# Optimization experiments

Hardware: AMD Instinct MI355X
Metric: run time of the kernel (lower is better)

Reference implementation:

```python
import jax, jax.numpy as jnp
import numpy as np


def _lstm_cell(x, h, c, Wih, Whh, bih, bhh):
    # PyTorch LSTMCell gate order: i, f, g, o
    g = x @ Wih.T + h @ Whh.T + bih + bhh
    i, f, gg, o = jnp.split(g, 4, axis=-1)
    c = jax.nn.sigmoid(f) * c + jax.nn.sigmoid(i) * jnp.tanh(gg)
    h = jax.nn.sigmoid(o) * jnp.tanh(c)
    return h, c


def setup_inputs() -> dict:
    F, H, B, Te, Td = 64, 128, 1024, 168, 24
    shapes = {
        'input_p_q': (B, Te, F), 'label_p': (B, Td),
        'Wi_w': (H, F), 'Wi_b': (H,), 'We_w': (H, 2 * H),
        'Vd_w': (F, H), 'Vd_b': (F,),
        'enc_Wih': (4 * H, F), 'enc_Whh': (4 * H, H), 'enc_bih': (4 * H,), 'enc_bhh': (4 * H,),
        'mid_Wih': (4 * H, H), 'mid_Whh': (4 * H, H), 'mid_bih': (4 * H,), 'mid_bhh': (4 * H,),
        'Wx_w': (H, H), 'Wx_b': (H,), 'Wh_w': (H, 2 * H),
        'V_w': (1, H), 'V_b': (1,),
        'dec_Wih': (4 * H, H), 'dec_Whh': (4 * H, H), 'dec_bih': (4 * H,), 'dec_bhh': (4 * H,),
        'reg_w': (1, H), 'reg_b': (1,),
    }
    key = jax.random.key(0)
    ks = jax.random.split(key, len(shapes))
    out = {}
    for k, (name, shp) in zip(ks, shapes.items()):
        scale = 1.0 if name in ('input_p_q', 'label_p') else 0.05
        out[name] = jax.random.normal(k, shp, jnp.float32) * scale
    return out


def reference(input_p_q, label_p, Wi_w, Wi_b, We_w, Vd_w, Vd_b,
              enc_Wih, enc_Whh, enc_bih, enc_bhh,
              mid_Wih, mid_Whh, mid_bih, mid_bhh,
              Wx_w, Wx_b, Wh_w, V_w, V_b,
              dec_Wih, dec_Whh, dec_bih, dec_bhh, reg_w, reg_b):
    B, Te, F = input_p_q.shape
    H = Wi_w.shape[0]
    Td = label_p.shape[1]
    h0 = jnp.zeros((B, H), input_p_q.dtype)

    # ---- spatial-attention LSTMCell encoder ----
    xs = jnp.transpose(input_p_q, (1, 0, 2))  # [Te, B, F]

    def enc_step(carry, x_t):
        h, c = carry
        s = jnp.tanh(jnp.concatenate([h, c], axis=1) @ We_w.T
                     + x_t @ Wi_w.T + Wi_b) @ Vd_w.T + Vd_b  # [B, F]
        x_in = x_t * jax.nn.softmax(s, axis=1)
        h, c = _lstm_cell(x_in, h, c, enc_Wih, enc_Whh, enc_bih, enc_bhh)
        return (h, c), h

    _, mid = jax.lax.scan(enc_step, (h0, h0), xs)  # [Te, B, H]

    # ---- single-layer nn.LSTM (LSTM_mid), zero init state ----
    def mid_step(carry, x_t):
        h, c = carry
        h, c = _lstm_cell(x_t, h, c, mid_Wih, mid_Whh, mid_bih, mid_bhh)
        return (h, c), h

    (hi, ci), mid_out = jax.lax.scan(mid_step, (h0, h0), mid)
    mid_out = jnp.transpose(mid_out, (1, 0, 2))  # [B, Te, H]

    # ---- temporal-attention LSTMCell decoder (no softmax on scores, faithful) ----
    wx_mid = mid_out @ Wx_w.T + Wx_b  # [B, Te, H]

    def dec_step(carry, _):
        hi, ci = carry
        q = jnp.concatenate([hi, ci], axis=1) @ Wh_w.T  # [B, H]
        s = jnp.tanh(q[:, None, :] + wx_mid) @ V_w.T + V_b  # [B, Te, 1]
        dec_in = jnp.einsum('bt,bth->bh', s[..., 0], mid_out)
        hi, ci = _lstm_cell(dec_in, hi, ci, dec_Wih, dec_Whh, dec_bih, dec_bhh)
        return (hi, ci), hi

    _, dec = jax.lax.scan(dec_step, (hi, ci), None, length=Td)  # [Td, B, H]
    out = jnp.transpose(dec, (1, 0, 2)) @ reg_w.T + reg_b  # [B, Td, 1]
    return out[..., 0]
```

## Files before the change

### kernel.cpp

```cpp
#include <hip/hip_runtime.h>

#define B_   1024
#define TE   168
#define TD   24
#define F_   64
#define H_   128
#define H2_  256
#define G_   512

#define OFF_WhT    0
#define OFF_dWihT  16384
#define OFF_dWhhT  49152
#define OFF_ENCB   81920
#define OFF_MIDB   82432
#define OFF_DECB   82944
#define OFF_W16    83456
#define W16_We     0
#define W16_Wi     32768
#define W16_Vd     40960
#define W16_eWih   49152
#define W16_eWhh   81920
#define W16_mWih   147456
#define W16_mWhh   212992
#define W16_Wx     278528
#define W16_TOT    294912
#define OFF_MID    230912
#define OFF_WX     (OFF_MID + (B_*TE*H_)/2)
#define OFF_STH    (OFF_WX  + (B_*TE*H_)/2)
#define OFF_STC    (OFF_STH + B_*H_)
#define WS_FLOATS  (OFF_STC + B_*H_)

typedef _Float16 h2 __attribute__((ext_vector_type(2)));
typedef _Float16 h8 __attribute__((ext_vector_type(8)));
typedef _Float16 f16x8 __attribute__((ext_vector_type(8)));
typedef float    f32x4 __attribute__((ext_vector_type(4)));

__device__ __forceinline__ float fexp2(float x) { return __builtin_amdgcn_exp2f(x); }
__device__ __forceinline__ float frcp(float x)  { return __builtin_amdgcn_rcpf(x); }
#define LOG2E 1.4426950408889634f

__device__ __forceinline__ float sigm(float x) {
    return frcp(1.f + fexp2(-LOG2E * x));
}
__device__ __forceinline__ float tanh_fast(float x) {
    float e = fexp2(2.f * LOG2E * x);
    return 1.f - 2.f * frcp(e + 1.f);
}

__device__ __forceinline__ float fdot2(h2 a, h2 b, float c) {
#if __has_builtin(__builtin_amdgcn_fdot2)
    return __builtin_amdgcn_fdot2(a, b, c, false);
#else
    return c + (float)a[0] * (float)b[0] + (float)a[1] * (float)b[1];
#endif
}
__device__ __forceinline__ void fma4(float4& g, const float4 wv, const float s) {
    g.x = __builtin_fmaf(wv.x, s, g.x);
    g.y = __builtin_fmaf(wv.y, s, g.y);
    g.z = __builtin_fmaf(wv.z, s, g.z);
    g.w = __builtin_fmaf(wv.w, s, g.w);
}

#define SH(V,I)  __builtin_shufflevector(V, V, 2*(I), 2*(I)+1)
#define SL(CG)   (4*((CG) + ((CG)>>3)))

#define DPAIR2(LOV, HIV, R0, R1) { \
    h2 c0=SH(LOV,0), c1=SH(LOV,1), c2=SH(LOV,2), c3=SH(LOV,3); \
    h2 c4=SH(HIV,0), c5=SH(HIV,1), c6=SH(HIV,2), c7=SH(HIV,3); \
    a00.x=fdot2(R0,c0,a00.x); a00.y=fdot2(R0,c1,a00.y); a00.z=fdot2(R0,c2,a00.z); a00.w=fdot2(R0,c3,a00.w); \
    a01.x=fdot2(R0,c4,a01.x); a01.y=fdot2(R0,c5,a01.y); a01.z=fdot2(R0,c6,a01.z); a01.w=fdot2(R0,c7,a01.w); \
    a10.x=fdot2(R1,c0,a10.x); a10.y=fdot2(R1,c1,a10.y); a10.z=fdot2(R1,c2,a10.z); a10.w=fdot2(R1,c3,a10.w); \
    a11.x=fdot2(R1,c4,a11.x); a11.y=fdot2(R1,c5,a11.y); a11.z=fdot2(R1,c6,a11.z); a11.w=fdot2(R1,c7,a11.w); \
}

__device__ __forceinline__ f32x4 mfma16(f16x8 a, f16x8 b, f32x4 c) {
    return __builtin_amdgcn_mfma_f32_16x16x32_f16(a, b, c, 0, 0, 0);
}

struct PrepArgs {
    const float *We, *Wi, *Vd, *eWih, *eWhh, *eBih, *eBhh,
                *mWih, *mWhh, *mBih, *mBhh, *Wx, *Wh, *dWih, *dWhh, *dBih, *dBhh;
};

__global__ void prep_kernel(PrepArgs a, float* __restrict__ ws) {
    int sec  = blockIdx.x >> 2;
    int base = (blockIdx.x & 3) * blockDim.x + threadIdx.x;
    const int stride = blockDim.x * 4;
    _Float16* w16 = (_Float16*)(ws + OFF_W16);

    if (sec <= 2) {
        const float* src = (sec == 0) ? a.Wh : (sec == 1) ? a.dWih : a.dWhh;
        int R = (sec == 0) ? 128 : 512;
        int C = (sec == 0) ? 256 : 128;
        int off = (sec == 0) ? OFF_WhT : (sec == 1) ? OFF_dWihT : OFF_dWhhT;
        int n = R * C;
        _Float16* hd = (_Float16*)(ws + off);
        for (int o = base; o < n; o += stride) {
            int r = o % R, c = o / R;
            hd[(c >> 1) * 2 * R + 2 * r + (c & 1)] = (_Float16)src[r * C + c];
        }
    } else if (sec == 3) {
        for (int i = base; i < 512; i += stride) ws[OFF_ENCB + i] = a.eBih[i] + a.eBhh[i];
    } else if (sec == 4) {
        for (int i = base; i < 512; i += stride) ws[OFF_MIDB + i] = a.mBih[i] + a.mBhh[i];
    } else if (sec == 5) {
        for (int i = base; i < 512; i += stride) ws[OFF_DECB + i] = a.dBih[i] + a.dBhh[i];
    } else if (sec <= 13) {
        const int dsto[8] = {W16_We, W16_Wi, W16_Vd, W16_eWih, W16_eWhh, W16_mWih, W16_mWhh, W16_Wx};
        const int cnt[8]  = {32768, 8192, 8192, 32768, 65536, 65536, 65536, 16384};
        const float* srcs[8] = {a.We, a.Wi, a.Vd, a.eWih, a.eWhh, a.mWih, a.mWhh, a.Wx};
        int k = sec - 6;
        const float* s = srcs[k];
        _Float16* d = w16 + dsto[k];
        int n = cnt[k];
        for (int i = base; i < n; i += stride) d[i] = (_Float16)s[i];
    }
}

__global__ __launch_bounds__(512, 1) void enc_kernel(
    const float* __restrict__ x_all,
    const float* __restrict__ Wi_b,
    const float* __restrict__ Vd_b,
    float* __restrict__ ws)
{
    __shared__ __align__(16) _Float16 m1In[16][328];
    __shared__ __align__(16) _Float16 encIn[16][200];
    __shared__ __align__(16) _Float16 avT[16][136];
    __shared__ __align__(16) float sS[16][68];
    __shared__ __align__(16) float xf[16][64];
    __shared__ __align__(16) float cE[16][132];
    __shared__ float bWi[H_], bVd[F_], bE[G_];

    const int tid  = threadIdx.x;
    const int wave = tid >> 6;
    const int lane = tid & 63;
    const int g    = lane >> 4;
    const int cc   = lane & 15;
    const int b0   = blockIdx.x * 16;
    const int col  = wave * 16 + cc;

    for (int i = tid; i < 16 * 328; i += 512) ((_Float16*)m1In)[i]  = (_Float16)0.f;
    for (int i = tid; i < 16 * 200; i += 512) ((_Float16*)encIn)[i] = (_Float16)0.f;
    for (int i = tid; i < 16 * 132; i += 512) ((float*)cE)[i] = 0.f;
    if (tid < H_) bWi[tid] = Wi_b[tid];
    if (tid < F_) bVd[tid] = Vd_b[tid];
    bE[tid] = ws[OFF_ENCB + tid];
    if (tid < 256) {
        int m = tid >> 4, c4 = (tid & 15) * 4;
        float4 v = *(const float4*)&x_all[((size_t)(b0 + m) * TE + 0) * F_ + c4];
        *(float4*)&xf[m][c4] = v;
        m1In[m][256 + c4]     = (_Float16)v.x;
        m1In[m][256 + c4 + 1] = (_Float16)v.y;
        m1In[m][256 + c4 + 2] = (_Float16)v.z;
        m1In[m][256 + c4 + 3] = (_Float16)v.w;
    }

    const _Float16* w16 = (const _Float16*)(ws + OFF_W16);
    f16x8 wWe[8], wWi[2], wVd[4], wIh[4][2], wHh[4][4];
    {
        const _Float16* p = w16 + W16_We + (size_t)col * 256 + 8 * g;
        #pragma unroll
        for (int ks = 0; ks < 8; ++ks) wWe[ks] = *(const f16x8*)(p + ks * 32);
        const _Float16* p2 = w16 + W16_Wi + (size_t)col * 64 + 8 * g;
        wWi[0] = *(const f16x8*)(p2);
        wWi[1] = *(const f16x8*)(p2 + 32);
        if (wave < 4) {
            const _Float16* p3 = w16 + W16_Vd + (size_t)col * 128 + 8 * g;
            #pragma unroll
            for (int ks = 0; ks < 4; ++ks) wVd[ks] = *(const f16x8*)(p3 + ks * 32);
        } else {
            #pragma unroll
            for (int ks = 0; ks < 4; ++ks) wVd[ks] = f16x8{};
        }
        #pragma unroll
        for (int q = 0; q < 4; ++q) {
            const _Float16* pi = w16 + W16_eWih + (size_t)(q * 128 + col) * 64 + 8 * g;
            wIh[q][0] = *(const f16x8*)(pi);
            wIh[q][1] = *(const f16x8*)(pi + 32);
            const _Float16* ph = w16 + W16_eWhh + (size_t)(q * 128 + col) * 128 + 8 * g;
            #pragma unroll
            for (int ks = 0; ks < 4; ++ks) wHh[q][ks] = *(const f16x8*)(ph + ks * 32);
        }
    }
    _Float16* hencG = (_Float16*)(ws + OFF_MID);
    __syncthreads();

    float4 xr = make_float4(0.f, 0.f, 0.f, 0.f);

    for (int t = 0; t < TE; ++t) {
        {
            f16x8 aF[10];
            #pragma unroll
            for (int ks = 0; ks < 10; ++ks)
                aF[ks] = *(const f16x8*)&m1In[cc][ks * 32 + 8 * g];
            f32x4 acc = {0.f, 0.f, 0.f, 0.f};
            #pragma unroll
            for (int ks = 0; ks < 8; ++ks)
                acc = mfma16(aF[ks], wWe[ks], acc);
            acc = mfma16(aF[8], wWi[0], acc);
            acc = mfma16(aF[9], wWi[1], acc);
            float bw = bWi[col];
            #pragma unroll
            for (int r = 0; r < 4; ++r)
                avT[4 * g + r][col] = (_Float16)tanh_fast(acc[r] + bw);
        }
        __syncthreads();

        if (wave < 4) {
            f16x8 aF[4];
            #pragma unroll
            for (int ks = 0; ks < 4; ++ks)
                aF[ks] = *(const f16x8*)&avT[cc][ks * 32 + 8 * g];
            f32x4 acc = {0.f, 0.f, 0.f, 0.f};
            #pragma unroll
            for (int ks = 0; ks < 4; ++ks)
                acc = mfma16(aF[ks], wVd[ks], acc);
            float bv = bVd[col];
            #pragma unroll
            for (int r = 0; r < 4; ++r)
                sS[4 * g + r][col] = acc[r] + bv;
        } else if (t + 1 < TE) {
            int q = tid - 256, m = q >> 4, c4 = (q & 15) * 4;
            xr = *(const float4*)&x_all[((size_t)(b0 + m) * TE + (t + 1)) * F_ + c4];
        }
        __syncthreads();

        {
            int m = tid >> 5, c = tid & 31;
            float v0 = sS[m][c], v1 = sS[m][c + 32];
            float mx = fmaxf(v0, v1);
            #pragma unroll
            for (int off = 16; off > 0; off >>= 1) mx = fmaxf(mx, __shfl_xor(mx, off, 64));
            float e0 = fexp2((v0 - mx) * LOG2E);
            float e1 = fexp2((v1 - mx) * LOG2E);
            float sm = e0 + e1;
            #pragma unroll
            for (int off = 16; off > 0; off >>= 1) sm += __shfl_xor(sm, off, 64);
            float rs = frcp(sm);
            encIn[m][c]      = (_Float16)(xf[m][c]      * e0 * rs);
            encIn[m][c + 32] = (_Float16)(xf[m][c + 32] * e1 * rs);
        }
        __syncthreads();

        f32x4 ge[4];
        {
            f16x8 aF[6];
            #pragma unroll
            for (int ks = 0; ks < 6; ++ks)
                aF[ks] = *(const f16x8*)&encIn[cc][ks * 32 + 8 * g];
            #pragma unroll
            for (int q = 0; q < 4; ++q) {
                f32x4 acc = {0.f, 0.f, 0.f, 0.f};
                acc = mfma16(aF[0], wIh[q][0], acc);
                acc = mfma16(aF[1], wIh[q][1], acc);
                #pragma unroll
                for (int ks = 0; ks < 4; ++ks)
                    acc = mfma16(aF[2 + ks], wHh[q][ks], acc);
                ge[q] = acc;
            }
        }
        __syncthreads();
        {
            float bi = bE[col], bf = bE[col + 128], bg = bE[col + 256], bo = bE[col + 384];
            #pragma unroll
            for (int r = 0; r < 4; ++r) {
                int m = 4 * g + r;
                float gi = ge[0][r] + bi, gf = ge[1][r] + bf,
                      gg = ge[2][r] + bg, go = ge[3][r] + bo;
                float cn = sigm(gf) * cE[m][col] + sigm(gi) * tanh_fast(gg);
                float h  = sigm(go) * tanh_fast(cn);
                cE[m][col] = cn;
                _Float16 hh = (_Float16)h;
                encIn[m][64 + col] = hh;
                m1In[m][col]       = hh;
                m1In[m][128 + col] = (_Float16)cn;
                hencG[((size_t)(b0 + m) * TE + t) * H_ + col] = hh;
            }
            if (tid >= 256 && t + 1 < TE) {
                int q = tid - 256, m = q >> 4, c4 = (q & 15) * 4;
                *(float4*)&xf[m][c4] = xr;
                m1In[m][256 + c4]     = (_Float16)xr.x;
                m1In[m][256 + c4 + 1] = (_Float16)xr.y;
                m1In[m][256 + c4 + 2] = (_Float16)xr.z;
                m1In[m][256 + c4 + 3] = (_Float16)xr.w;
            }
        }
        __syncthreads();
    }
}

__global__ __launch_bounds__(512, 1) void mid_kernel(
    const float* __restrict__ Wx_b,
    float* __restrict__ ws)
{
    __shared__ __align__(16) _Float16 midIn[16][264];
    __shared__ __align__(16) float cM[16][132];
    __shared__ float bM[G_], bWx[H_];

    const int tid  = threadIdx.x;
    const int wave = tid >> 6;
    const int lane = tid & 63;
    const int g    = lane >> 4;
    const int cc   = lane & 15;
    const int b0   = blockIdx.x * 16;
    const int col  = wave * 16 + cc;

    for (int i = tid; i < 16 * 264; i += 512) ((_Float16*)midIn)[i] = (_Float16)0.f;
    for (int i = tid; i < 16 * 132; i += 512) ((float*)cM)[i] = 0.f;
    if (tid < H_) bWx[tid] = Wx_b[tid];
    bM[tid] = ws[OFF_MIDB + tid];

    const _Float16* w16 = (const _Float16*)(ws + OFF_W16);
    f16x8 wIhB[4][4], wHhB[4][4], wWx[4];
    {
        #pragma unroll
        for (int q = 0; q < 4; ++q) {
            const _Float16* pi = w16 + W16_mWih + (size_t)(q * 128 + col) * 128 + 8 * g;
            const _Float16* ph = w16 + W16_mWhh + (size_t)(q * 128 + col) * 128 + 8 * g;
            #pragma unroll
            for (int ks = 0; ks < 4; ++ks) {
                wIhB[q][ks] = *(const f16x8*)(pi + ks * 32);
                wHhB[q][ks] = *(const f16x8*)(ph + ks * 32);
            }
        }
        const _Float16* px = w16 + W16_Wx + (size_t)col * 128 + 8 * g;
        #pragma unroll
        for (int ks = 0; ks < 4; ++ks) wWx[ks] = *(const f16x8*)(px + ks * 32);
    }

    _Float16* hencG = (_Float16*)(ws + OFF_MID);
    _Float16* wxH   = (_Float16*)(ws + OFF_WX);
    __syncthreads();

    if (tid < 256) {
        int m = tid >> 4, s8 = (tid & 15) * 8;
        *(f16x8*)&midIn[m][s8] = *(const f16x8*)&hencG[((size_t)(b0 + m) * TE + 0) * H_ + s8];
    }
    __syncthreads();

    f16x8 hpre = {};
    f32x4 accx = {0.f, 0.f, 0.f, 0.f};

    for (int t = 0; t < TE; ++t) {
        f32x4 gm[4];
        {
            f16x8 aF[8];
            #pragma unroll
            for (int ks = 0; ks < 8; ++ks)
                aF[ks] = *(const f16x8*)&midIn[cc][ks * 32 + 8 * g];
            #pragma unroll
            for (int q = 0; q < 4; ++q) {
                f32x4 acc = {0.f, 0.f, 0.f, 0.f};
                #pragma unroll
                for (int ks = 0; ks < 4; ++ks)
                    acc = mfma16(aF[ks], wIhB[q][ks], acc);
                #pragma unroll
                for (int ks = 0; ks < 4; ++ks)
                    acc = mfma16(aF[4 + ks], wHhB[q][ks], acc);
                gm[q] = acc;
            }
            if (t > 0) {
                f32x4 acc = {0.f, 0.f, 0.f, 0.f};
                #pragma unroll
                for (int ks = 0; ks < 4; ++ks)
                    acc = mfma16(aF[4 + ks], wWx[ks], acc);
                accx = acc;
            }
        }
        if (tid < 256 && t + 1 < TE) {
            int m = tid >> 4, s8 = (tid & 15) * 8;
            hpre = *(const f16x8*)&hencG[((size_t)(b0 + m) * TE + (t + 1)) * H_ + s8];
        }
        __syncthreads();

        {
            float bi = bM[col], bf = bM[col + 128], bg = bM[col + 256], bo = bM[col + 384];
            float bw = bWx[col];
            #pragma unroll
            for (int r = 0; r < 4; ++r) {
                int m = 4 * g + r;
                float gi = gm[0][r] + bi, gf = gm[1][r] + bf,
                      gg = gm[2][r] + bg, go = gm[3][r] + bo;
                float cn = sigm(gf) * cM[m][col] + sigm(gi) * tanh_fast(gg);
                float h  = sigm(go) * tanh_fast(cn);
                cM[m][col] = cn;
                _Float16 hh = (_Float16)h;
                midIn[m][128 + col] = hh;
                hencG[((size_t)(b0 + m) * TE + t) * H_ + col] = hh;
                if (t > 0)
                    wxH[((size_t)(b0 + m) * TE + (t - 1)) * H_ + col] = (_Float16)(accx[r] + bw);
            }
            if (tid < 256 && t + 1 < TE) {
                int m = tid >> 4, s8 = (tid & 15) * 8;
                *(f16x8*)&midIn[m][s8] = hpre;
            }
        }
        __syncthreads();
    }

    {
        f16x8 ax[4];
        #pragma unroll
        for (int ks = 0; ks < 4; ++ks)
            ax[ks] = *(const f16x8*)&midIn[cc][128 + ks * 32 + 8 * g];
        f32x4 acc = {0.f, 0.f, 0.f, 0.f};
        #pragma unroll
        for (int ks = 0; ks < 4; ++ks)
            acc = mfma16(ax[ks], wWx[ks], acc);
        float bw = bWx[col];
        #pragma unroll
        for (int r = 0; r < 4; ++r) {
            int m = 4 * g + r;
            wxH[((size_t)(b0 + m) * TE + (TE - 1)) * H_ + col] = (_Float16)(acc[r] + bw);
        }
    }
    for (int idx = tid; idx < 2048; idx += 512) {
        int m = idx >> 7, j = idx & 127;
        ws[OFF_STH + (b0 + m) * H_ + j] = (float)midIn[m][128 + j];
        ws[OFF_STC + (b0 + m) * H_ + j] = cM[m][j];
    }
}

#define QP_ 132

__global__ __launch_bounds__(512, 2) void dec_kernel(
    const float* __restrict__ Vw_in,
    const float* __restrict__ Vb_in,
    const float* __restrict__ rw_in,
    const float* __restrict__ rb_in,
    const float* __restrict__ ws,
    float* __restrict__ out)
{
    __shared__ __align__(16) float scr[9216];
    __shared__ __align__(16) float hc2[2][H2_];
    __shared__ __align__(16) float qv[2][QP_];
    __shared__ __align__(16) float sb[2][TE];
    __shared__ __align__(16) float dinp[8][2][H_];
    __shared__ float bD[G_], Vw[H_], rw[H_];

    const int tid = threadIdx.x;
    const int b0  = blockIdx.x * 2;
    const float Vb = Vb_in[0], rb = rb_in[0];

    {
        int r = tid >> 8, c = tid & 255;
        hc2[r][c] = (c < H_) ? ws[OFF_STH + (b0 + r) * H_ + c]
                             : ws[OFF_STC + (b0 + r) * H_ + (c - H_)];
    }
    if (tid < H_) { Vw[tid] = Vw_in[tid]; rw[tid] = rw_in[tid]; }
    bD[tid] = ws[OFF_DECB + tid];
    __syncthreads();

    const h8* WhH2  = (const h8*)(ws + OFF_WhT);
    const h8* dWih2 = (const h8*)(ws + OFF_dWihT);
    const h8* dWhh2 = (const h8*)(ws + OFF_dWhhT);
    const h8* wx8   = (const h8*)(ws + OFF_WX);
    typedef _Float16 h4 __attribute__((ext_vector_type(4)));
    const h4* mid4 = (const h4*)(ws + OFF_MID);

    for (int td = 0; td < TD; ++td) {
        {
            int cg = tid & 15, ks = tid >> 4;
            int p0 = ks * 4;
            float4 a00 = make_float4(0.f,0.f,0.f,0.f), a01 = a00, a10 = a00, a11 = a00;
            #pragma unroll
            for (int i = 0; i < 4; ++i) {
                int p = p0 + i;
                h8 lo = WhH2[p * 32 + cg * 2];
                h8 hi = WhH2[p * 32 + cg * 2 + 1];
                h2 r0; r0[0] = (_Float16)hc2[0][2*p]; r0[1] = (_Float16)hc2[0][2*p+1];
                h2 r1; r1[0] = (_Float16)hc2[1][2*p]; r1[1] = (_Float16)hc2[1][2*p+1];
                DPAIR2(lo, hi, r0, r1);
            }
            int sl = SL(cg);
            float* sp = scr + ks * 288;
            *(float4*)(sp +       sl) = a00; *(float4*)(sp +  72 + sl) = a01;
            *(float4*)(sp + 144 + sl) = a10; *(float4*)(sp + 216 + sl) = a11;
        }
        __syncthreads();
        if (tid < 256) {
            int j = tid & 127, r = tid >> 7;
            int e = j & 7, cgj = j >> 3;
            int idx = r * 144 + ((e < 4) ? SL(cgj) + e : 72 + SL(cgj) + (e - 4));
            float v = 0.f;
            #pragma unroll
            for (int ks = 0; ks < 32; ++ks) v += scr[ks * 288 + idx];
            qv[r][j] = v;
        }
        __syncthreads();

        for (int task = tid; task < 2 * TE; task += 512) {
            int r = (task >= TE) ? 1 : 0;
            int tp = task - r * TE;
            const h8* wxr = wx8 + ((size_t)(b0 + r) * TE + tp) * 16;
            float acc = Vb;
            #pragma unroll 4
            for (int kk = 0; kk < 16; ++kk) {
                h8 hv = wxr[kk];
                int j = kk * 8;
                float4 q0 = *(const float4*)&qv[r][j], q1 = *(const float4*)&qv[r][j + 4];
                float4 v0 = *(const float4*)&Vw[j],    v1 = *(const float4*)&Vw[j + 4];
                acc += tanh_fast(q0.x + (float)hv[0]) * v0.x + tanh_fast(q0.y + (float)hv[1]) * v0.y
                     + tanh_fast(q0.z + (float)hv[2]) * v0.z + tanh_fast(q0.w + (float)hv[3]) * v0.w;
                acc += tanh_fast(q1.x + (float)hv[4]) * v1.x + tanh_fast(q1.y + (float)hv[5]) * v1.y
                     + tanh_fast(q1.z + (float)hv[6]) * v1.z + tanh_fast(q1.w + (float)hv[7]) * v1.w;
            }
            sb[r][tp] = acc;
        }
        __syncthreads();

        {
            int ts = tid >> 6, r = (tid >> 5) & 1, cg = tid & 31;
            int t0 = ts * 21;
            float4 a = make_float4(0.f, 0.f, 0.f, 0.f);
            #pragma unroll 3
            for (int tp = t0; tp < t0 + 21; ++tp) {
                float s = sb[r][tp];
                h4 m = mid4[((size_t)(b0 + r) * TE + tp) * 32 + cg];
                float4 mf;
                mf.x = (float)m[0]; mf.y = (float)m[1]; mf.z = (float)m[2]; mf.w = (float)m[3];
                fma4(a, mf, s);
            }
            *(float4*)&dinp[ts][r][cg * 4] = a;
        }
        __syncthreads();
        if (tid < 256) {
            int j = tid & 127, r = tid >> 7;
            qv[r][j] = ((dinp[0][r][j] + dinp[1][r][j]) + (dinp[2][r][j] + dinp[3][r][j]))
                     + ((dinp[4][r][j] + dinp[5][r][j]) + (dinp[6][r][j] + dinp[7][r][j]));
        }
        __syncthreads();

        {
            int cg = tid & 63, ks = tid >> 6;
            int p0 = ks * 8;
            float4 a00 = make_float4(0.f,0.f,0.f,0.f), a01 = a00, a10 = a00, a11 = a00;
            #pragma unroll 4
            for (int i = 0; i < 8; ++i) {
                int p = p0 + i;
                h8 lo = dWih2[p * 128 + cg * 2];
                h8 hi = dWih2[p * 128 + cg * 2 + 1];
                h2 r0; r0[0] = (_Float16)qv[0][2*p]; r0[1] = (_Float16)qv[0][2*p+1];
                h2 r1; r1[0] = (_Float16)qv[1][2*p]; r1[1] = (_Float16)qv[1][2*p+1];
                DPAIR2(lo, hi, r0, r1);
            }
            #pragma unroll 4
            for (int i = 0; i < 8; ++i) {
                int p = p0 + i;
                h8 lo = dWhh2[p * 128 + cg * 2];
                h8 hi = dWhh2[p * 128 + cg * 2 + 1];
                h2 r0; r0[0] = (_Float16)hc2[0][2*p]; r0[1] = (_Float16)hc2[0][2*p+1];
                h2 r1; r1[0] = (_Float16)hc2[1][2*p]; r1[1] = (_Float16)hc2[1][2*p+1];
                DPAIR2(lo, hi, r0, r1);
            }
            int sl = SL(cg);
            float* sp = scr + ks * 1152;
            *(float4*)(sp +       sl) = a00; *(float4*)(sp + 288 + sl) = a01;
            *(float4*)(sp + 576 + sl) = a10; *(float4*)(sp + 864 + sl) = a11;
        }
        __syncthreads();

        if (tid < 256) {
            int j = tid & 127, r = tid >> 7;
            int e = j & 7, cgj = j >> 3;
            int i0, i1, i2, i3;
            {
                int c0 = cgj, c1 = 16 + cgj, c2 = 32 + cgj, c3 = 48 + cgj;
                i0 = (e < 4) ? SL(c0) + e : 288 + SL(c0) + (e - 4);
                i1 = (e < 4) ? SL(c1) + e : 288 + SL(c1) + (e - 4);
                i2 = (e < 4) ? SL(c2) + e : 288 + SL(c2) + (e - 4);
                i3 = (e < 4) ? SL(c3) + e : 288 + SL(c3) + (e - 4);
            }
            const float* sp = scr + r * 576;
            float gi = bD[j], gf = bD[j + 128], gg = bD[j + 256], go = bD[j + 384];
            #pragma unroll
            for (int ks = 0; ks < 8; ++ks) {
                const float* p = sp + ks * 1152;
                gi += p[i0]; gf += p[i1]; gg += p[i2]; go += p[i3];
            }
            float c = sigm(gf) * hc2[r][H_ + j] + sigm(gi) * tanh_fast(gg);
            float h = sigm(go) * tanh_fast(c);
            hc2[r][H_ + j] = c; hc2[r][j] = h;
        }
        __syncthreads();

        if (tid < 128) {
            int r = tid >> 6, lane = tid & 63;
            float v = hc2[r][lane] * rw[lane] + hc2[r][lane + 64] * rw[lane + 64];
            for (int off = 32; off > 0; off >>= 1) v += __shfl_xor(v, off, 64);
            if (lane == 0) out[(b0 + r) * TD + td] = v + rb;
        }
    }
}

extern "C" void kernel_launch(void* const* d_in, const int* in_sizes, int n_in,
                              void* d_out, int out_size, void* d_ws, size_t ws_size,
                              hipStream_t stream)
{
    (void)in_sizes; (void)n_in; (void)out_size;
    if (ws_size < (size_t)WS_FLOATS * sizeof(float)) return;

    const float* x_all = (const float*)d_in[0];
    const float* Wi_b  = (const float*)d_in[3];
    const float* Vd_b  = (const float*)d_in[6];
    const float* Wx_b  = (const float*)d_in[16];
    const float* V_w   = (const float*)d_in[18];
    const float* V_b   = (const float*)d_in[19];
    const float* reg_w = (const float*)d_in[24];
    const float* reg_b = (const float*)d_in[25];
    float* ws  = (float*)d_ws;
    float* out = (float*)d_out;

    PrepArgs pa{
        (const float*)d_in[4],
        (const float*)d_in[2],
        (const float*)d_in[5],
        (const float*)d_in[7],
        (const float*)d_in[8],
        (const float*)d_in[9],
        (const float*)d_in[10],
        (const float*)d_in[11],
        (const float*)d_in[12],
        (const float*)d_in[13],
        (const float*)d_in[14],
        (const float*)d_in[15],
        (const float*)d_in[17],
        (const float*)d_in[20],
        (const float*)d_in[21],
        (const float*)d_in[22],
        (const float*)d_in[23]
    };

    prep_kernel<<<56, 256, 0, stream>>>(pa, ws);
    enc_kernel<<<64, 512, 0, stream>>>(x_all, Wi_b, Vd_b, ws);
    mid_kernel<<<64, 512, 0, stream>>>(Wx_b, ws);
    dec_kernel<<<512, 512, 0, stream>>>(V_w, V_b, reg_w, reg_b, ws, out);
}
```

Measured before the change: 1.288 ms.

## Restructure decoder to one batch row per block with register-resident weights

```diff
diff --git a/kernel.cpp b/kernel.cpp
--- a/kernel.cpp
+++ b/kernel.cpp
@@ -31,7 +31,6 @@
 #define WS_FLOATS  (OFF_STC + B_*H_)
 
 typedef _Float16 h2 __attribute__((ext_vector_type(2)));
-typedef _Float16 h8 __attribute__((ext_vector_type(8)));
 typedef _Float16 f16x8 __attribute__((ext_vector_type(8)));
 typedef float    f32x4 __attribute__((ext_vector_type(4)));
 
@@ -54,23 +53,13 @@
     return c + (float)a[0] * (float)b[0] + (float)a[1] * (float)b[1];
 #endif
 }
-__device__ __forceinline__ void fma4(float4& g, const float4 wv, const float s) {
-    g.x = __builtin_fmaf(wv.x, s, g.x);
-    g.y = __builtin_fmaf(wv.y, s, g.y);
-    g.z = __builtin_fmaf(wv.z, s, g.z);
-    g.w = __builtin_fmaf(wv.w, s, g.w);
-}
 
 #define SH(V,I)  __builtin_shufflevector(V, V, 2*(I), 2*(I)+1)
-#define SL(CG)   (4*((CG) + ((CG)>>3)))
-
-#define DPAIR2(LOV, HIV, R0, R1) { \
-    h2 c0=SH(LOV,0), c1=SH(LOV,1), c2=SH(LOV,2), c3=SH(LOV,3); \
-    h2 c4=SH(HIV,0), c5=SH(HIV,1), c6=SH(HIV,2), c7=SH(HIV,3); \
-    a00.x=fdot2(R0,c0,a00.x); a00.y=fdot2(R0,c1,a00.y); a00.z=fdot2(R0,c2,a00.z); a00.w=fdot2(R0,c3,a00.w); \
-    a01.x=fdot2(R0,c4,a01.x); a01.y=fdot2(R0,c5,a01.y); a01.z=fdot2(R0,c6,a01.z); a01.w=fdot2(R0,c7,a01.w); \
-    a10.x=fdot2(R1,c0,a10.x); a10.y=fdot2(R1,c1,a10.y); a10.z=fdot2(R1,c2,a10.z); a10.w=fdot2(R1,c3,a10.w); \
-    a11.x=fdot2(R1,c4,a11.x); a11.y=fdot2(R1,c5,a11.y); a11.z=fdot2(R1,c6,a11.z); a11.w=fdot2(R1,c7,a11.w); \
+#define DOT8(ACC, HV, WV) { \
+    ACC = fdot2(SH(HV,0), SH(WV,0), ACC); \
+    ACC = fdot2(SH(HV,1), SH(WV,1), ACC); \
+    ACC = fdot2(SH(HV,2), SH(WV,2), ACC); \
+    ACC = fdot2(SH(HV,3), SH(WV,3), ACC); \
 }
 
 __device__ __forceinline__ f32x4 mfma16(f16x8 a, f16x8 b, f32x4 c) {
@@ -90,15 +79,10 @@
 
     if (sec <= 2) {
         const float* src = (sec == 0) ? a.Wh : (sec == 1) ? a.dWih : a.dWhh;
-        int R = (sec == 0) ? 128 : 512;
-        int C = (sec == 0) ? 256 : 128;
+        int n = (sec == 0) ? 32768 : 65536;
         int off = (sec == 0) ? OFF_WhT : (sec == 1) ? OFF_dWihT : OFF_dWhhT;
-        int n = R * C;
         _Float16* hd = (_Float16*)(ws + off);
-        for (int o = base; o < n; o += stride) {
-            int r = o % R, c = o / R;
-            hd[(c >> 1) * 2 * R + 2 * r + (c & 1)] = (_Float16)src[r * C + c];
-        }
+        for (int o = base; o < n; o += stride) hd[o] = (_Float16)src[o];
     } else if (sec == 3) {
         for (int i = base; i < 512; i += stride) ws[OFF_ENCB + i] = a.eBih[i] + a.eBhh[i];
     } else if (sec == 4) {
@@ -421,9 +405,7 @@
     }
 }
 
-#define QP_ 132
-
-__global__ __launch_bounds__(512, 2) void dec_kernel(
+__global__ __launch_bounds__(512, 1) void dec_kernel(
     const float* __restrict__ Vw_in,
     const float* __restrict__ Vb_in,
     const float* __restrict__ rw_in,
@@ -431,164 +413,148 @@
     const float* __restrict__ ws,
     float* __restrict__ out)
 {
-    __shared__ __align__(16) float scr[9216];
-    __shared__ __align__(16) float hc2[2][H2_];
-    __shared__ __align__(16) float qv[2][QP_];
-    __shared__ __align__(16) float sb[2][TE];
-    __shared__ __align__(16) float dinp[8][2][H_];
-    __shared__ float bD[G_], Vw[H_], rw[H_];
+    __shared__ __align__(16) _Float16 wxL[TE][136];
+    __shared__ __align__(16) _Float16 midL[TE][136];
+    __shared__ __align__(16) _Float16 hcH[H2_];
+    __shared__ __align__(16) _Float16 dinH[H_];
+    __shared__ __align__(16) float hF[H_];
+    __shared__ __align__(16) float cD[H_];
+    __shared__ __align__(16) float qv[H_];
+    __shared__ __align__(16) float sv[TE];
+    __shared__ __align__(16) float dpart[4][H_];
+    __shared__ __align__(16) float ggs[G_];
+    __shared__ float bDL[G_], VwL[H_], rwL[H_];
 
     const int tid = threadIdx.x;
-    const int b0  = blockIdx.x * 2;
+    const int b   = blockIdx.x;
     const float Vb = Vb_in[0], rb = rb_in[0];
 
+    const _Float16* Wh16  = (const _Float16*)(ws + OFF_WhT);
+    const _Float16* dIh16 = (const _Float16*)(ws + OFF_dWihT);
+    const _Float16* dHh16 = (const _Float16*)(ws + OFF_dWhhT);
+    const int j1  = tid >> 2;
+    const int ks1 = tid & 3;
+
+    f16x8 wWh[8], wIh[16], wHh[16];
     {
-        int r = tid >> 8, c = tid & 255;
-        hc2[r][c] = (c < H_) ? ws[OFF_STH + (b0 + r) * H_ + c]
-                             : ws[OFF_STC + (b0 + r) * H_ + (c - H_)];
-    }
-    if (tid < H_) { Vw[tid] = Vw_in[tid]; rw[tid] = rw_in[tid]; }
-    bD[tid] = ws[OFF_DECB + tid];
+        const _Float16* p = Wh16 + (size_t)j1 * 256 + ks1 * 64;
+        #pragma unroll
+        for (int k = 0; k < 8; ++k) wWh[k] = *(const f16x8*)(p + k * 8);
+        const _Float16* pi = dIh16 + (size_t)tid * 128;
+        const _Float16* ph = dHh16 + (size_t)tid * 128;
+        #pragma unroll
+        for (int k = 0; k < 16; ++k) {
+            wIh[k] = *(const f16x8*)(pi + k * 8);
+            wHh[k] = *(const f16x8*)(ph + k * 8);
+        }
+    }
+
+    {
+        const _Float16* wxG  = (const _Float16*)(ws + OFF_WX)  + (size_t)b * TE * H_;
+        const _Float16* midG = (const _Float16*)(ws + OFF_MID) + (size_t)b * TE * H_;
+        for (int i = tid; i < TE * 16; i += 512) {
+            int tp = i >> 4, c8 = (i & 15) * 8;
+            *(f16x8*)&wxL[tp][c8]  = *(const f16x8*)(wxG  + (size_t)tp * H_ + c8);
+            *(f16x8*)&midL[tp][c8] = *(const f16x8*)(midG + (size_t)tp * H_ + c8);
+        }
+    }
+    if (tid < 128) {
+        float sh = ws[OFF_STH + (size_t)b * H_ + tid];
+        float sc = ws[OFF_STC + (size_t)b * H_ + tid];
+        hcH[tid]       = (_Float16)sh;
+        hcH[128 + tid] = (_Float16)sc;
+        cD[tid] = sc;
+        VwL[tid] = Vw_in[tid];
+        rwL[tid] = rw_in[tid];
+    }
+    bDL[tid] = ws[OFF_DECB + tid];
     __syncthreads();
 
-    const h8* WhH2  = (const h8*)(ws + OFF_WhT);
-    const h8* dWih2 = (const h8*)(ws + OFF_dWihT);
-    const h8* dWhh2 = (const h8*)(ws + OFF_dWhhT);
-    const h8* wx8   = (const h8*)(ws + OFF_WX);
-    typedef _Float16 h4 __attribute__((ext_vector_type(4)));
-    const h4* mid4 = (const h4*)(ws + OFF_MID);
-
     for (int td = 0; td < TD; ++td) {
         {
-            int cg = tid & 15, ks = tid >> 4;
-            int p0 = ks * 4;
-            float4 a00 = make_float4(0.f,0.f,0.f,0.f), a01 = a00, a10 = a00, a11 = a00;
-            #pragma unroll
-            for (int i = 0; i < 4; ++i) {
-                int p = p0 + i;
-                h8 lo = WhH2[p * 32 + cg * 2];
-                h8 hi = WhH2[p * 32 + cg * 2 + 1];
-                h2 r0; r0[0] = (_Float16)hc2[0][2*p]; r0[1] = (_Float16)hc2[0][2*p+1];
-                h2 r1; r1[0] = (_Float16)hc2[1][2*p]; r1[1] = (_Float16)hc2[1][2*p+1];
-                DPAIR2(lo, hi, r0, r1);
-            }
-            int sl = SL(cg);
-            float* sp = scr + ks * 288;
-            *(float4*)(sp +       sl) = a00; *(float4*)(sp +  72 + sl) = a01;
-            *(float4*)(sp + 144 + sl) = a10; *(float4*)(sp + 216 + sl) = a11;
-        }
-        __syncthreads();
-        if (tid < 256) {
-            int j = tid & 127, r = tid >> 7;
-            int e = j & 7, cgj = j >> 3;
-            int idx = r * 144 + ((e < 4) ? SL(cgj) + e : 72 + SL(cgj) + (e - 4));
-            float v = 0.f;
-            #pragma unroll
-            for (int ks = 0; ks < 32; ++ks) v += scr[ks * 288 + idx];
-            qv[r][j] = v;
-        }
-        __syncthreads();
-
-        for (int task = tid; task < 2 * TE; task += 512) {
-            int r = (task >= TE) ? 1 : 0;
-            int tp = task - r * TE;
-            const h8* wxr = wx8 + ((size_t)(b0 + r) * TE + tp) * 16;
-            float acc = Vb;
+            const _Float16* hp = hcH + ks1 * 64;
+            float acc = 0.f;
+            #pragma unroll
+            for (int k8 = 0; k8 < 8; ++k8) {
+                f16x8 hv = *(const f16x8*)(hp + k8 * 8);
+                DOT8(acc, hv, wWh[k8]);
+            }
+            acc += __shfl_xor(acc, 1, 64);
+            acc += __shfl_xor(acc, 2, 64);
+            if (ks1 == 0) qv[j1] = acc;
+        }
+        __syncthreads();
+
+        if (tid < 2 * TE) {
+            int tp = tid >> 1, hf = tid & 1;
+            const _Float16* wxp = &wxL[tp][hf * 64];
+            const float* qp = qv + hf * 64;
+            const float* vp = VwL + hf * 64;
+            float acc = 0.f;
             #pragma unroll 4
-            for (int kk = 0; kk < 16; ++kk) {
-                h8 hv = wxr[kk];
-                int j = kk * 8;
-                float4 q0 = *(const float4*)&qv[r][j], q1 = *(const float4*)&qv[r][j + 4];
-                float4 v0 = *(const float4*)&Vw[j],    v1 = *(const float4*)&Vw[j + 4];
-                acc += tanh_fast(q0.x + (float)hv[0]) * v0.x + tanh_fast(q0.y + (float)hv[1]) * v0.y
-                     + tanh_fast(q0.z + (float)hv[2]) * v0.z + tanh_fast(q0.w + (float)hv[3]) * v0.w;
-                acc += tanh_fast(q1.x + (float)hv[4]) * v1.x + tanh_fast(q1.y + (float)hv[5]) * v1.y
-                     + tanh_fast(q1.z + (float)hv[6]) * v1.z + tanh_fast(q1.w + (float)hv[7]) * v1.w;
-            }
-            sb[r][tp] = acc;
-        }
-        __syncthreads();
-
-        {
-            int ts = tid >> 6, r = (tid >> 5) & 1, cg = tid & 31;
-            int t0 = ts * 21;
-            float4 a = make_float4(0.f, 0.f, 0.f, 0.f);
-            #pragma unroll 3
-            for (int tp = t0; tp < t0 + 21; ++tp) {
-                float s = sb[r][tp];
-                h4 m = mid4[((size_t)(b0 + r) * TE + tp) * 32 + cg];
-                float4 mf;
-                mf.x = (float)m[0]; mf.y = (float)m[1]; mf.z = (float)m[2]; mf.w = (float)m[3];
-                fma4(a, mf, s);
-            }
-            *(float4*)&dinp[ts][r][cg * 4] = a;
-        }
-        __syncthreads();
-        if (tid < 256) {
-            int j = tid & 127, r = tid >> 7;
-            qv[r][j] = ((dinp[0][r][j] + dinp[1][r][j]) + (dinp[2][r][j] + dinp[3][r][j]))
-                     + ((dinp[4][r][j] + dinp[5][r][j]) + (dinp[6][r][j] + dinp[7][r][j]));
-        }
-        __syncthreads();
-
-        {
-            int cg = tid & 63, ks = tid >> 6;
-            int p0 = ks * 8;
-            float4 a00 = make_float4(0.f,0.f,0.f,0.f), a01 = a00, a10 = a00, a11 = a00;
-            #pragma unroll 4
-            for (int i = 0; i < 8; ++i) {
-                int p = p0 + i;
-                h8 lo = dWih2[p * 128 + cg * 2];
-                h8 hi = dWih2[p * 128 + cg * 2 + 1];
-                h2 r0; r0[0] = (_Float16)qv[0][2*p]; r0[1] = (_Float16)qv[0][2*p+1];
-                h2 r1; r1[0] = (_Float16)qv[1][2*p]; r1[1] = (_Float16)qv[1][2*p+1];
-                DPAIR2(lo, hi, r0, r1);
-            }
-            #pragma unroll 4
-            for (int i = 0; i < 8; ++i) {
-                int p = p0 + i;
-                h8 lo = dWhh2[p * 128 + cg * 2];
-                h8 hi = dWhh2[p * 128 + cg * 2 + 1];
-                h2 r0; r0[0] = (_Float16)hc2[0][2*p]; r0[1] = (_Float16)hc2[0][2*p+1];
-                h2 r1; r1[0] = (_Float16)hc2[1][2*p]; r1[1] = (_Float16)hc2[1][2*p+1];
-                DPAIR2(lo, hi, r0, r1);
-            }
-            int sl = SL(cg);
-            float* sp = scr + ks * 1152;
-            *(float4*)(sp +       sl) = a00; *(float4*)(sp + 288 + sl) = a01;
-            *(float4*)(sp + 576 + sl) = a10; *(float4*)(sp + 864 + sl) = a11;
-        }
-        __syncthreads();
-
-        if (tid < 256) {
-            int j = tid & 127, r = tid >> 7;
-            int e = j & 7, cgj = j >> 3;
-            int i0, i1, i2, i3;
-            {
-                int c0 = cgj, c1 = 16 + cgj, c2 = 32 + cgj, c3 = 48 + cgj;
-                i0 = (e < 4) ? SL(c0) + e : 288 + SL(c0) + (e - 4);
-                i1 = (e < 4) ? SL(c1) + e : 288 + SL(c1) + (e - 4);
-                i2 = (e < 4) ? SL(c2) + e : 288 + SL(c2) + (e - 4);
-                i3 = (e < 4) ? SL(c3) + e : 288 + SL(c3) + (e - 4);
-            }
-            const float* sp = scr + r * 576;
-            float gi = bD[j], gf = bD[j + 128], gg = bD[j + 256], go = bD[j + 384];
-            #pragma unroll
-            for (int ks = 0; ks < 8; ++ks) {
-                const float* p = sp + ks * 1152;
-                gi += p[i0]; gf += p[i1]; gg += p[i2]; go += p[i3];
-            }
-            float c = sigm(gf) * hc2[r][H_ + j] + sigm(gi) * tanh_fast(gg);
-            float h = sigm(go) * tanh_fast(c);
-            hc2[r][H_ + j] = c; hc2[r][j] = h;
-        }
-        __syncthreads();
-
+            for (int k8 = 0; k8 < 8; ++k8) {
+                f16x8 wv = *(const f16x8*)(wxp + k8 * 8);
+                float4 q0 = *(const float4*)(qp + k8 * 8);
+                float4 q1 = *(const float4*)(qp + k8 * 8 + 4);
+                float4 v0 = *(const float4*)(vp + k8 * 8);
+                float4 v1 = *(const float4*)(vp + k8 * 8 + 4);
+                acc += tanh_fast(q0.x + (float)wv[0]) * v0.x + tanh_fast(q0.y + (float)wv[1]) * v0.y
+                     + tanh_fast(q0.z + (float)wv[2]) * v0.z + tanh_fast(q0.w + (float)wv[3]) * v0.w;
+                acc += tanh_fast(q1.x + (float)wv[4]) * v1.x + tanh_fast(q1.y + (float)wv[5]) * v1.y
+                     + tanh_fast(q1.z + (float)wv[6]) * v1.z + tanh_fast(q1.w + (float)wv[7]) * v1.w;
+            }
+            acc += __shfl_xor(acc, 1, 64);
+            if (hf == 0) sv[tp] = acc + Vb;
+        }
+        __syncthreads();
+
+        {
+            int j = tid & 127, sl = tid >> 7;
+            int t0 = sl * 42;
+            float acc = 0.f;
+            for (int tp = t0; tp < t0 + 42; ++tp)
+                acc = __builtin_fmaf(sv[tp], (float)midL[tp][j], acc);
+            dpart[sl][j] = acc;
+        }
+        __syncthreads();
         if (tid < 128) {
-            int r = tid >> 6, lane = tid & 63;
-            float v = hc2[r][lane] * rw[lane] + hc2[r][lane + 64] * rw[lane + 64];
+            float d = (dpart[0][tid] + dpart[1][tid]) + (dpart[2][tid] + dpart[3][tid]);
+            dinH[tid] = (_Float16)d;
+        }
+        __syncthreads();
+
+        {
+            float acc = bDL[tid];
+            #pragma unroll 8
+            for (int k8 = 0; k8 < 16; ++k8) {
+                f16x8 dv = *(const f16x8*)(dinH + k8 * 8);
+                DOT8(acc, dv, wIh[k8]);
+            }
+            #pragma unroll 8
+            for (int k8 = 0; k8 < 16; ++k8) {
+                f16x8 hv = *(const f16x8*)(hcH + k8 * 8);
+                DOT8(acc, hv, wHh[k8]);
+            }
+            ggs[tid] = acc;
+        }
+        __syncthreads();
+
+        if (tid < 128) {
+            float gi = ggs[tid], gf = ggs[tid + 128], gg = ggs[tid + 256], go = ggs[tid + 384];
+            float cn = sigm(gf) * cD[tid] + sigm(gi) * tanh_fast(gg);
+            float h  = sigm(go) * tanh_fast(cn);
+            cD[tid] = cn;
+            hF[tid] = h;
+            hcH[tid]       = (_Float16)h;
+            hcH[128 + tid] = (_Float16)cn;
+        }
+        __syncthreads();
+
+        if (tid < 64) {
+            float v = hF[tid] * rwL[tid] + hF[tid + 64] * rwL[tid + 64];
+            #pragma unroll
             for (int off = 32; off > 0; off >>= 1) v += __shfl_xor(v, off, 64);
-            if (lane == 0) out[(b0 + r) * TD + td] = v + rb;
+            if (tid == 0) out[(size_t)b * TD + td] = v + rb;
         }
     }
 }
@@ -634,5 +600,5 @@
     prep_kernel<<<56, 256, 0, stream>>>(pa, ws);
     enc_kernel<<<64, 512, 0, stream>>>(x_all, Wi_b, Vd_b, ws);
     mid_kernel<<<64, 512, 0, stream>>>(Wx_b, ws);
-    dec_kernel<<<512, 512, 0, stream>>>(V_w, V_b, reg_w, reg_b, ws, out);
-}
+    dec_kernel<<<1024, 512, 0, stream>>>(V_w, V_b, reg_w, reg_b, ws, out);
+}
```

After: 2.002 ms. 55.4% more time.
